# Kernel optimization log

Measured on AMD Instinct MI355X. Metric: run time of the kernel, lower is better.

The kernel has to match this reference:

```python
import jax, jax.numpy as jnp
import numpy as np

S = (128, 128, 128)  # spatial grid
K = (16, 16, 16)     # retained low-frequency modes


def _gelu(x):
    # torch nn.GELU default = exact erf variant
    return jax.nn.gelu(x, approximate=False)


def _flayer(x, Rr, Ri, w):
    # x: (s1,s2,s3,dv). Full rfftn then truncate to low modes (as in source).
    f = jnp.fft.rfftn(x, axes=(0, 1, 2))[: K[0], : K[1], : K[2]]  # (k1,k2,k3,dv) complex
    Rf = jnp.einsum('abcd,abcde->abce', f, Rr + 1j * Ri)           # per-mode channel mix
    kernelpart = jnp.fft.irfftn(Rf, s=S, axes=(0, 1, 2))           # zero-pad modes, back to grid
    return _gelu(kernelpart + x @ w)


def setup_inputs() -> dict:
    key = jax.random.key(0)
    ks = jax.random.split(key, 20)
    da, dv, dout = 4, 32, 1
    sc1, sc2, sc3 = 2.0 / da, 2.0 / dv, 2.0 / dv
    d = {}
    d['x'] = jax.random.normal(ks[0], (*S, da), dtype=jnp.float32)
    d['win'] = sc1 * jax.random.normal(ks[1], (da, dv), dtype=jnp.float32)
    d['bin1'] = sc1 * jax.random.normal(ks[2], (dv,), dtype=jnp.float32)
    i = 3
    for L in range(1, 5):
        d[f'Rphir{L}'] = sc2 * jax.random.normal(ks[i], (*K, dv, dv), dtype=jnp.float32); i += 1
        d[f'Rphii{L}'] = sc2 * jax.random.normal(ks[i], (*K, dv, dv), dtype=jnp.float32); i += 1
        d[f'w{L}'] = sc2 * jax.random.normal(ks[i], (dv, dv), dtype=jnp.float32); i += 1
    d['wout'] = sc3 * jax.random.normal(ks[i], (dv, dout), dtype=jnp.float32); i += 1
    d['bout'] = sc3 * jax.random.normal(ks[i], (dout,), dtype=jnp.float32)
    return d


def reference(x, win, bin1, Rphir1, Rphii1, w1, Rphir2, Rphii2, w2,
              Rphir3, Rphii3, w3, Rphir4, Rphii4, w4, wout, bout):
    v = _gelu(x @ win + bin1)          # lifting: (s1,s2,s3,dv)
    v = _flayer(v, Rphir1, Rphii1, w1)
    v = _flayer(v, Rphir2, Rphii2, w2)
    v = _flayer(v, Rphir3, Rphii3, w3)
    v = _flayer(v, Rphir4, Rphii4, w4)
    return v @ wout + bout             # (s1,s2,s3,dout)
```

## Files before the change

### kernel.cpp

```cpp
#include <hip/hip_runtime.h>
#include <math.h>

typedef float2 cplx;
typedef _Float16 h16;
typedef h16 h16x8 __attribute__((ext_vector_type(8)));
typedef float f32x4 __attribute__((ext_vector_type(4)));
typedef uint u32x2 __attribute__((ext_vector_type(2)));

#define MFMA16(a, b, c) __builtin_amdgcn_mfma_f32_16x16x32_f16(a, b, c, 0, 0, 0)

static __device__ __forceinline__ float gelu_exact(float z) {
  float x = z * 0.70710678118654752440f;
  float ax = fabsf(x);
  float t = __builtin_amdgcn_rcpf(fmaf(0.3275911f, ax, 1.0f));
  float p = fmaf(1.061405429f, t, -1.453152027f);
  p = fmaf(p, t, 1.421413741f);
  p = fmaf(p, t, -0.284496736f);
  p = fmaf(p, t, 0.254829592f);
  p = p * t;
  float e = __expf(-ax * ax);
  float erfax = fmaf(-p, e, 1.0f);
  float er = copysignf(erfax, x);
  return 0.5f * z * (1.0f + er);
}

template <int OFF>
static __device__ __forceinline__ h16x8 tr_frag(uint addr) {
  union { uint u[4]; h16x8 h; } r;
  u32x2 lo, hi;
  asm volatile("ds_read_b64_tr_b16 %0, %2 offset:%3\n\t"
               "ds_read_b64_tr_b16 %1, %2 offset:%4"
               : "=&v"(lo), "=&v"(hi)
               : "v"(addr), "i"(OFF), "i"(OFF + 128));
  r.u[0] = lo.x; r.u[1] = lo.y; r.u[2] = hi.x; r.u[3] = hi.y;
  return r.h;
}

__global__ __launch_bounds__(256) void k_prep(
    h16* __restrict__ Afwd, h16* __restrict__ Adt, cplx* __restrict__ Twc,
    const float* __restrict__ wA, const float* __restrict__ wB,
    const float* __restrict__ wC, h16* __restrict__ Wfr)
{
  const int tid = threadIdx.x;
  const float w0 = 0.049087385212340519f;
  for (int idx = tid; idx < 4096; idx += 256) {
    int Mt = idx >> 11, rem = idx & 2047, lane = rem >> 5, k = rem & 31;
    int j = k & 7, chunk = k >> 3;
    int m = lane & 15;
    int x3 = chunk * 32 + (lane >> 4) * 8 + j;
    float ang = (float)((m * x3) & 127) * w0;
    float s, c; sincosf(ang, &s, &c);
    float val = Mt ? s : c;
    h16 hi = (h16)val;
    Afwd[idx] = hi;
    Afwd[idx + 4096] = (h16)(val - (float)hi);
  }
  for (int idx = tid; idx < 4096; idx += 256) {
    int tt = idx >> 4, rem = idx & 15, t = rem >> 3, j = rem & 7;
    int wv = tt >> 6, lane = tt & 63, mrow = lane & 15, q = lane >> 4;
    int x3 = (2 * wv + t) * 16 + mrow;
    int kk = q * 8 + j;
    int m = (kk < 16) ? kk : kk - 16;
    float ang = (float)((x3 * m) & 127) * w0;
    float s, c; sincosf(ang, &s, &c);
    Adt[idx] = (h16)((kk < 16) ? c : s);
  }
  const float* ws[3] = { wA, wB, wC };
  for (int idx = tid; idx < 12288; idx += 256) {
    int L = idx >> 12, rem = idx & 4095;
    int t2 = rem >> 4, nt = (rem >> 3) & 1, j = rem & 7;
    int mrow = t2 & 15, q = (t2 >> 4) & 3;
    int n = nt * 16 + mrow, kk = q * 8 + j;
    Wfr[idx] = (h16)ws[L][kk * 32 + n];
  }
  if (tid < 128) {
    float ang = (float)tid * w0;
    float s, c; sincosf(ang, &s, &c);
    Twc[tid] = make_float2(c, s);
  }
}

__global__ __launch_bounds__(256) void k_lift(
    const float* __restrict__ x, const float* __restrict__ win,
    const float* __restrict__ bin, h16* __restrict__ v)
{
  __shared__ float xr[512];
  __shared__ float wl[128];
  __shared__ float bl[32];
  const int tid = threadIdx.x;
  const size_t b = blockIdx.x;
  const float* xrow = x + b * 512;
  for (int i = tid; i < 512; i += 256) xr[i] = xrow[i];
  if (tid < 128) wl[tid] = win[tid];
  if (tid < 32)  bl[tid] = bin[tid];
  __syncthreads();
  const int c = tid & 31, g = tid >> 5;
  #pragma unroll
  for (int j = 0; j < 16; ++j) {
    int x3 = g + 8 * j;
    float z = bl[c];
    #pragma unroll
    for (int a = 0; a < 4; ++a) z += xr[x3 * 4 + a] * wl[a * 32 + c];
    v[b * 4096 + x3 * 32 + c] = (h16)gelu_exact(z);
  }
}

__global__ __launch_bounds__(256) void k_fwd3(
    const h16* __restrict__ v, const h16* __restrict__ Afwd, cplx* __restrict__ Gp,
    const cplx* __restrict__ twg)
{
  __shared__ __align__(16) h16 vtile[4][2][4][32][16];
  __shared__ cplx F3L[4][512];
  __shared__ cplx twc[128];
  const int tid = threadIdx.x;
  const int x1 = blockIdx.x, qs = blockIdx.y;
  if (tid < 128) twc[tid] = twg[tid];
  const int lane = tid & 63, wv = tid >> 6;
  const int mrow = lane & 15, q4 = lane >> 4;
  h16x8 Ah[2][4], Al[2][4];
  #pragma unroll
  for (int Mt = 0; Mt < 2; ++Mt)
    #pragma unroll
    for (int ch = 0; ch < 4; ++ch) {
      Ah[Mt][ch] = *(const h16x8*)&Afwd[Mt * 2048 + lane * 32 + ch * 8];
      Al[Mt][ch] = *(const h16x8*)&Afwd[4096 + Mt * 2048 + lane * 32 + ch * 8];
    }
  const uint ldsbase = (uint)(uintptr_t)&vtile[0][0][0][0][0];
  const uint abase = ldsbase + (uint)(wv * 8192 + q4 * 256 + mrow * 2);
  cplx g0[16], g1[16];
  #pragma unroll
  for (int k2 = 0; k2 < 16; ++k2) { g0[k2] = make_float2(0.f, 0.f); g1[k2] = make_float2(0.f, 0.f); }
  for (int it = 0; it < 8; ++it) {
    const int x2b = qs * 32 + it * 4;
    __syncthreads();
    const uint4* vsrc = (const uint4*)(v + ((size_t)x1 * 128 + x2b) * 4096);
    for (int i = tid; i < 2048; i += 256) {
      uint4 pk = vsrc[i];
      int rr = i >> 9, e = (i & 511) * 8, x3 = e >> 5, c0 = e & 31;
      int panel = c0 >> 4, off = c0 & 15;
      int chunk = x3 >> 5, row = x3 & 31;
      *(uint4*)&vtile[rr][panel][chunk][row][off] = pk;
    }
    __syncthreads();
    h16x8 B0[4], B1[4];
    {
      const uint a0 = abase;
      const uint a1 = abase + 4096;
      B0[0] = tr_frag<0>(a0);    B0[1] = tr_frag<1024>(a0);
      B0[2] = tr_frag<2048>(a0); B0[3] = tr_frag<3072>(a0);
      B1[0] = tr_frag<0>(a1);    B1[1] = tr_frag<1024>(a1);
      B1[2] = tr_frag<2048>(a1); B1[3] = tr_frag<3072>(a1);
      asm volatile("s_waitcnt lgkmcnt(0)" ::: "memory");
      __builtin_amdgcn_sched_barrier(0);
    }
    f32x4 acc[2][2];
    #pragma unroll
    for (int Mt = 0; Mt < 2; ++Mt)
      #pragma unroll
      for (int Nt = 0; Nt < 2; ++Nt) acc[Mt][Nt] = (f32x4){0.f, 0.f, 0.f, 0.f};
    #pragma unroll
    for (int ch = 0; ch < 4; ++ch) {
      acc[0][0] = MFMA16(Ah[0][ch], B0[ch], acc[0][0]);
      acc[0][0] = MFMA16(Al[0][ch], B0[ch], acc[0][0]);
      acc[0][1] = MFMA16(Ah[0][ch], B1[ch], acc[0][1]);
      acc[0][1] = MFMA16(Al[0][ch], B1[ch], acc[0][1]);
      acc[1][0] = MFMA16(Ah[1][ch], B0[ch], acc[1][0]);
      acc[1][0] = MFMA16(Al[1][ch], B0[ch], acc[1][0]);
      acc[1][1] = MFMA16(Ah[1][ch], B1[ch], acc[1][1]);
      acc[1][1] = MFMA16(Al[1][ch], B1[ch], acc[1][1]);
    }
    #pragma unroll
    for (int Nt = 0; Nt < 2; ++Nt)
      #pragma unroll
      for (int r = 0; r < 4; ++r)
        F3L[wv][(q4 * 4 + r) * 32 + Nt * 16 + mrow] =
            make_float2(acc[0][Nt][r], -acc[1][Nt][r]);
    __syncthreads();
    #pragma unroll
    for (int rr = 0; rr < 4; ++rr) {
      const int x2 = x2b + rr;
      cplx f0 = F3L[rr][tid], f1 = F3L[rr][tid + 256];
      #pragma unroll
      for (int k2 = 0; k2 < 16; ++k2) {
        cplx t = twc[(k2 * x2) & 127];
        g0[k2].x += f0.x * t.x + f0.y * t.y;  g0[k2].y += f0.y * t.x - f0.x * t.y;
        g1[k2].x += f1.x * t.x + f1.y * t.y;  g1[k2].y += f1.y * t.x - f1.x * t.y;
      }
    }
  }
  cplx* dst = Gp + (size_t)qs * 1048576;
  #pragma unroll
  for (int k2 = 0; k2 < 16; ++k2) {
    size_t base = ((size_t)x1 * 16 + k2) * 512;
    dst[base + tid] = g0[k2];
    dst[base + 256 + tid] = g1[k2];
  }
}

__global__ __launch_bounds__(256) void k_spec(
    const cplx* __restrict__ Gp, const float* __restrict__ Rr,
    const float* __restrict__ Ri, cplx* __restrict__ H1,
    const cplx* __restrict__ twg)
{
  __shared__ cplx twc[128];
  __shared__ cplx fb[512];
  __shared__ cplx tb[512];
  const int tid = threadIdx.x;
  const int k2 = blockIdx.x >> 4, k3 = blockIdx.x & 15;
  if (tid < 128) twc[tid] = twg[tid];
  __syncthreads();
  const int c = tid & 31, g = tid >> 5;
  float fr0 = 0.f, fi0 = 0.f, fr1 = 0.f, fi1 = 0.f;
  for (int x1 = 0; x1 < 128; ++x1) {
    size_t idx = (((size_t)x1 * 16 + k2) * 16 + k3) * 32 + c;
    cplx p0 = Gp[idx], p1 = Gp[idx + 1048576], p2 = Gp[idx + 2097152], p3 = Gp[idx + 3145728];
    cplx h = make_float2(p0.x + p1.x + p2.x + p3.x, p0.y + p1.y + p2.y + p3.y);
    cplx ta = twc[(g * x1) & 127];
    cplx tb2 = twc[((g + 8) * x1) & 127];
    fr0 += h.x * ta.x + h.y * ta.y;   fi0 += h.y * ta.x - h.x * ta.y;
    fr1 += h.x * tb2.x + h.y * tb2.y; fi1 += h.y * tb2.x - h.x * tb2.y;
  }
  fb[g * 32 + c] = make_float2(fr0, fi0);
  fb[(g + 8) * 32 + c] = make_float2(fr1, fi1);
  __syncthreads();
  {
    const int e = c;
    float tr0 = 0.f, ti0 = 0.f, tr1 = 0.f, ti1 = 0.f;
    const size_t mb0 = ((size_t)g * 256 + k2 * 16 + k3) * 1024;
    const size_t mb1 = ((size_t)(g + 8) * 256 + k2 * 16 + k3) * 1024;
    #pragma unroll 4
    for (int cc = 0; cc < 32; ++cc) {
      float rr0 = Rr[mb0 + cc * 32 + e], ri0 = Ri[mb0 + cc * 32 + e];
      float rr1 = Rr[mb1 + cc * 32 + e], ri1 = Ri[mb1 + cc * 32 + e];
      cplx f0 = fb[g * 32 + cc], f1 = fb[(g + 8) * 32 + cc];
      tr0 += f0.x * rr0 - f0.y * ri0;  ti0 += f0.x * ri0 + f0.y * rr0;
      tr1 += f1.x * rr1 - f1.y * ri1;  ti1 += f1.x * ri1 + f1.y * rr1;
    }
    const float s = 4.76837158203125e-07f;
    tb[g * 32 + e] = make_float2(tr0 * s, ti0 * s);
    tb[(g + 8) * 32 + e] = make_float2(tr1 * s, ti1 * s);
  }
  __syncthreads();
  float trr[16], tii[16];
  #pragma unroll
  for (int k1 = 0; k1 < 16; ++k1) { cplx t = tb[k1 * 32 + c]; trr[k1] = t.x; tii[k1] = t.y; }
  #pragma unroll
  for (int j = 0; j < 16; ++j) {
    int xx1 = g + 8 * j;
    float hr = 0.f, hi = 0.f;
    #pragma unroll
    for (int k1 = 0; k1 < 16; ++k1) {
      cplx t = twc[(k1 * xx1) & 127];
      hr += trr[k1] * t.x - tii[k1] * t.y;
      hi += trr[k1] * t.y + tii[k1] * t.x;
    }
    H1[(((size_t)xx1 * 16 + k2) * 16 + k3) * 32 + c] = make_float2(hr, hi);
  }
}

__global__ __launch_bounds__(256) void k_ptm2(
    const cplx* __restrict__ H1, const h16* __restrict__ Wfr,
    h16* __restrict__ v, const h16* __restrict__ Adt,
    const cplx* __restrict__ twg)
{
  __shared__ __align__(16) h16 St[2][32 * 40];
  const int tid = threadIdx.x;
  const int x1 = blockIdx.y;
  const int x2b = blockIdx.x * 8;
  const int c = tid & 31, g = tid >> 5;
  const int lane = tid & 63, wv = tid >> 6;
  const int mrow = lane & 15, q = lane >> 4;
  h16x8 Adf[2], Bw[2];
  Adf[0] = *(const h16x8*)&Adt[tid * 16];
  Adf[1] = *(const h16x8*)&Adt[tid * 16 + 8];
  Bw[0]  = *(const h16x8*)&Wfr[tid * 16];
  Bw[1]  = *(const h16x8*)&Wfr[tid * 16 + 8];
  cplx h1a[16], h1b[16];
  {
    const cplx* h1p = H1 + (size_t)x1 * 8192;
    #pragma unroll
    for (int k2 = 0; k2 < 16; ++k2) {
      h1a[k2] = h1p[(k2 * 16 + g) * 32 + c];
      h1b[k2] = h1p[(k2 * 16 + g + 8) * 32 + c];
    }
  }
  for (int xi = 0; xi < 8; ++xi) {
    const int x2 = x2b + xi;
    const size_t b = (size_t)x1 * 128 + x2;
    h16x8 Av[2];
    #pragma unroll
    for (int t = 0; t < 2; ++t) {
      int x3 = (2 * wv + t) * 16 + mrow;
      Av[t] = *(const h16x8*)&v[b * 4096 + x3 * 32 + q * 8];
    }
    float r0 = 0.f, i0 = 0.f, r1 = 0.f, i1 = 0.f;
    #pragma unroll
    for (int k2 = 0; k2 < 16; ++k2) {
      cplx t = twg[(k2 * x2) & 127];
      r0 += h1a[k2].x * t.x - h1a[k2].y * t.y;  i0 += h1a[k2].x * t.y + h1a[k2].y * t.x;
      r1 += h1b[k2].x * t.x - h1b[k2].y * t.y;  i1 += h1b[k2].x * t.y + h1b[k2].y * t.x;
    }
    const float s0 = (g == 0) ? 1.f : 2.f;
    h16* stp = St[xi & 1];
    stp[c * 40 + g]      = (h16)(s0 * r0);
    stp[c * 40 + g + 8]  = (h16)(2.f * r1);
    stp[c * 40 + 16 + g] = (h16)(-s0 * i0);
    stp[c * 40 + 24 + g] = (h16)(-2.f * i1);
    __syncthreads();
    h16x8 Bst[2];
    #pragma unroll
    for (int nt = 0; nt < 2; ++nt)
      Bst[nt] = *(const h16x8*)&stp[(nt * 16 + mrow) * 40 + q * 8];
    f32x4 acc[2][2];
    #pragma unroll
    for (int t = 0; t < 2; ++t)
      #pragma unroll
      for (int nt = 0; nt < 2; ++nt) {
        f32x4 z = {0.f, 0.f, 0.f, 0.f};
        z = MFMA16(Adf[t], Bst[nt], z);
        z = MFMA16(Av[t], Bw[nt], z);
        acc[t][nt] = z;
      }
    #pragma unroll
    for (int t = 0; t < 2; ++t)
      #pragma unroll
      for (int nt = 0; nt < 2; ++nt)
        #pragma unroll
        for (int r = 0; r < 4; ++r) {
          int x3 = (2 * wv + t) * 16 + q * 4 + r;
          int cc = nt * 16 + mrow;
          v[b * 4096 + x3 * 32 + cc] = (h16)gelu_exact(acc[t][nt][r]);
        }
  }
}

__global__ __launch_bounds__(256) void k_ptf(
    const cplx* __restrict__ H1, const float* __restrict__ w,
    h16* __restrict__ v, const h16* __restrict__ Adt,
    const float* __restrict__ wout, const float* __restrict__ bout,
    float* __restrict__ out, const cplx* __restrict__ twg)
{
  __shared__ __align__(16) h16 vh[128 * 40];
  __shared__ __align__(16) h16 St[32 * 40];
  __shared__ __align__(16) h16 Wt[32 * 40];
  __shared__ cplx twc[128];
  __shared__ float wo[32];
  const int tid = threadIdx.x;
  const size_t b = blockIdx.x;
  const int x1 = (int)(b >> 7), x2 = (int)(b & 127);
  if (tid < 128) twc[tid] = twg[tid];
  {
    const uint* vg = (const uint*)(v + b * 4096);
    for (int i = tid; i < 2048; i += 256) {
      uint pk = vg[i];
      int e = 2 * i, r = e >> 5, cp = e & 31;
      *(uint*)&vh[r * 40 + cp] = pk;
    }
  }
  for (int i = tid; i < 1024; i += 256) {
    int k = i >> 5, n = i & 31;
    Wt[n * 40 + k] = (h16)w[i];
  }
  if (tid < 32) wo[tid] = wout[tid];
  __syncthreads();
  const int c = tid & 31, g = tid >> 5;
  {
    float r0 = 0.f, i0 = 0.f, r1 = 0.f, i1 = 0.f;
    const cplx* h1p = H1 + (size_t)x1 * 8192;
    #pragma unroll
    for (int k2 = 0; k2 < 16; ++k2) {
      cplx a  = h1p[(k2 * 16 + g) * 32 + c];
      cplx bb = h1p[(k2 * 16 + g + 8) * 32 + c];
      cplx t  = twc[(k2 * x2) & 127];
      r0 += a.x * t.x - a.y * t.y;   i0 += a.x * t.y + a.y * t.x;
      r1 += bb.x * t.x - bb.y * t.y; i1 += bb.x * t.y + bb.y * t.x;
    }
    const float s0 = (g == 0) ? 1.f : 2.f;
    St[c * 40 + g]        = (h16)(s0 * r0);
    St[c * 40 + g + 8]    = (h16)(2.f * r1);
    St[c * 40 + 16 + g]   = (h16)(-s0 * i0);
    St[c * 40 + 24 + g]   = (h16)(-2.f * i1);
  }
  const int lane = tid & 63, wv = tid >> 6;
  const int mrow = lane & 15, q = lane >> 4;
  h16x8 Adf[2];
  Adf[0] = *(const h16x8*)&Adt[tid * 16];
  Adf[1] = *(const h16x8*)&Adt[tid * 16 + 8];
  __syncthreads();
  h16x8 Bst[2], Bw[2], Av[2];
  #pragma unroll
  for (int nt = 0; nt < 2; ++nt) {
    int n = nt * 16 + mrow;
    Bst[nt] = *(const h16x8*)&St[n * 40 + q * 8];
    Bw[nt]  = *(const h16x8*)&Wt[n * 40 + q * 8];
  }
  #pragma unroll
  for (int t = 0; t < 2; ++t) {
    int x3 = (2 * wv + t) * 16 + mrow;
    Av[t] = *(const h16x8*)&vh[x3 * 40 + q * 8];
  }
  f32x4 acc[2][2];
  #pragma unroll
  for (int t = 0; t < 2; ++t)
    #pragma unroll
    for (int nt = 0; nt < 2; ++nt) {
      f32x4 z = {0.f, 0.f, 0.f, 0.f};
      z = MFMA16(Adf[t], Bst[nt], z);
      z = MFMA16(Av[t], Bw[nt], z);
      acc[t][nt] = z;
    }
  __syncthreads();
  #pragma unroll
  for (int t = 0; t < 2; ++t)
    #pragma unroll
    for (int nt = 0; nt < 2; ++nt)
      #pragma unroll
      for (int r = 0; r < 4; ++r) {
        int x3 = (2 * wv + t) * 16 + q * 4 + r;
        int cc = nt * 16 + mrow;
        vh[x3 * 40 + cc] = (h16)gelu_exact(acc[t][nt][r]);
      }
  __syncthreads();
  if (tid < 128) {
    float o = bout[0];
    #pragma unroll
    for (int cc = 0; cc < 32; ++cc) o += (float)vh[tid * 40 + cc] * wo[cc];
    out[b * 128 + tid] = o;
  }
}

__global__ void k_diag(float* out, float wsmb) {
  if (threadIdx.x == 0 && blockIdx.x == 0) out[0] = wsmb;
}

extern "C" void kernel_launch(void* const* d_in, const int* in_sizes, int n_in,
                              void* d_out, int out_size, void* d_ws, size_t ws_size,
                              hipStream_t stream)
{
  (void)in_sizes; (void)n_in; (void)out_size;
  const float* x    = (const float*)d_in[0];
  const float* win  = (const float*)d_in[1];
  const float* bin1 = (const float*)d_in[2];
  const float* Rr[4] = { (const float*)d_in[3], (const float*)d_in[6],
                         (const float*)d_in[9], (const float*)d_in[12] };
  const float* Ri[4] = { (const float*)d_in[4], (const float*)d_in[7],
                         (const float*)d_in[10], (const float*)d_in[13] };
  const float* wm[4] = { (const float*)d_in[5], (const float*)d_in[8],
                         (const float*)d_in[11], (const float*)d_in[14] };
  const float* wout = (const float*)d_in[15];
  const float* bout = (const float*)d_in[16];
  float* out = (float*)d_out;

  const size_t SZ_V  = 134217728;
  const size_t SZ_C  = 33554432;
  const size_t SZ_AF = 16384;
  const size_t SZ_AD = 8192;
  const size_t SZ_TW = 1024;
  const size_t SZ_WF = 24576;
  const size_t NEED = SZ_V + SZ_C + SZ_AF + SZ_AD + SZ_TW + SZ_WF;

  if (ws_size < NEED) {
    k_diag<<<1, 64, 0, stream>>>(out, (float)(ws_size >> 20));
    return;
  }
  char* p = (char*)d_ws;
  h16* v    = (h16*)p;  p += SZ_V;
  cplx* C   = (cplx*)p; p += SZ_C;
  h16* Afwd = (h16*)p;  p += SZ_AF;
  h16* Adt  = (h16*)p;  p += SZ_AD;
  cplx* Twc = (cplx*)p; p += SZ_TW;
  h16* Wfr  = (h16*)p;

  k_prep<<<1, 256, 0, stream>>>(Afwd, Adt, Twc, wm[0], wm[1], wm[2], Wfr);
  k_lift<<<16384, 256, 0, stream>>>(x, win, bin1, v);
  for (int L = 0; L < 4; ++L) {
    k_fwd3<<<dim3(128, 4), 256, 0, stream>>>(v, Afwd, C, Twc);
    k_spec<<<256, 256, 0, stream>>>(C, Rr[L], Ri[L], C, Twc);
    if (L < 3) k_ptm2<<<dim3(16, 128), 256, 0, stream>>>(C, Wfr + (size_t)L * 4096, v, Adt, Twc);
    else       k_ptf<<<16384, 256, 0, stream>>>(C, wm[3], v, Adt, wout, bout, out, Twc);
  }
}
```

Measured before the change: 848.1 us.

## Restructure final layer kernel to process eight rows per block with register-held spectra

The final pointwise/inverse-transform kernel now handles 8 x2 rows per block, loads the H1 spectral column into registers once, and reads v and the precomputed fp16 weight fragments directly from global memory instead of staging them through LDS. The output projection is fused into the MFMA epilogue through lane shuffles, which removes the LDS round-trip and two barriers. The launch grid drops from 16384 blocks to 2048. The spectral kernel's x1 loop also gets an unroll-4 pragma. The cost is higher register pressure and fewer, longer-running blocks.

```diff
diff --git a/kernel.cpp b/kernel.cpp
--- a/kernel.cpp
+++ b/kernel.cpp
@@ -39,7 +39,8 @@
 __global__ __launch_bounds__(256) void k_prep(
     h16* __restrict__ Afwd, h16* __restrict__ Adt, cplx* __restrict__ Twc,
     const float* __restrict__ wA, const float* __restrict__ wB,
-    const float* __restrict__ wC, h16* __restrict__ Wfr)
+    const float* __restrict__ wC, const float* __restrict__ wD,
+    h16* __restrict__ Wfr)
 {
   const int tid = threadIdx.x;
   const float w0 = 0.049087385212340519f;
@@ -65,8 +66,8 @@
     float s, c; sincosf(ang, &s, &c);
     Adt[idx] = (h16)((kk < 16) ? c : s);
   }
-  const float* ws[3] = { wA, wB, wC };
-  for (int idx = tid; idx < 12288; idx += 256) {
+  const float* ws[4] = { wA, wB, wC, wD };
+  for (int idx = tid; idx < 16384; idx += 256) {
     int L = idx >> 12, rem = idx & 4095;
     int t2 = rem >> 4, nt = (rem >> 3) & 1, j = rem & 7;
     int mrow = t2 & 15, q = (t2 >> 4) & 3;
@@ -211,6 +212,7 @@
   __syncthreads();
   const int c = tid & 31, g = tid >> 5;
   float fr0 = 0.f, fi0 = 0.f, fr1 = 0.f, fi1 = 0.f;
+  #pragma unroll 4
   for (int x1 = 0; x1 < 128; ++x1) {
     size_t idx = (((size_t)x1 * 16 + k2) * 16 + k3) * 32 + c;
     cplx p0 = Gp[idx], p1 = Gp[idx + 1048576], p2 = Gp[idx + 2097152], p3 = Gp[idx + 3145728];
@@ -334,98 +336,87 @@
   }
 }
 
-__global__ __launch_bounds__(256) void k_ptf(
-    const cplx* __restrict__ H1, const float* __restrict__ w,
-    h16* __restrict__ v, const h16* __restrict__ Adt,
+__global__ __launch_bounds__(256) void k_ptf2(
+    const cplx* __restrict__ H1, const h16* __restrict__ Wfr,
+    const h16* __restrict__ v, const h16* __restrict__ Adt,
     const float* __restrict__ wout, const float* __restrict__ bout,
     float* __restrict__ out, const cplx* __restrict__ twg)
 {
-  __shared__ __align__(16) h16 vh[128 * 40];
-  __shared__ __align__(16) h16 St[32 * 40];
-  __shared__ __align__(16) h16 Wt[32 * 40];
-  __shared__ cplx twc[128];
-  __shared__ float wo[32];
-  const int tid = threadIdx.x;
-  const size_t b = blockIdx.x;
-  const int x1 = (int)(b >> 7), x2 = (int)(b & 127);
-  if (tid < 128) twc[tid] = twg[tid];
-  {
-    const uint* vg = (const uint*)(v + b * 4096);
-    for (int i = tid; i < 2048; i += 256) {
-      uint pk = vg[i];
-      int e = 2 * i, r = e >> 5, cp = e & 31;
-      *(uint*)&vh[r * 40 + cp] = pk;
-    }
-  }
-  for (int i = tid; i < 1024; i += 256) {
-    int k = i >> 5, n = i & 31;
-    Wt[n * 40 + k] = (h16)w[i];
-  }
-  if (tid < 32) wo[tid] = wout[tid];
-  __syncthreads();
+  __shared__ __align__(16) h16 St[2][32 * 40];
+  const int tid = threadIdx.x;
+  const int x1 = blockIdx.y;
+  const int x2b = blockIdx.x * 8;
   const int c = tid & 31, g = tid >> 5;
-  {
-    float r0 = 0.f, i0 = 0.f, r1 = 0.f, i1 = 0.f;
-    const cplx* h1p = H1 + (size_t)x1 * 8192;
-    #pragma unroll
-    for (int k2 = 0; k2 < 16; ++k2) {
-      cplx a  = h1p[(k2 * 16 + g) * 32 + c];
-      cplx bb = h1p[(k2 * 16 + g + 8) * 32 + c];
-      cplx t  = twc[(k2 * x2) & 127];
-      r0 += a.x * t.x - a.y * t.y;   i0 += a.x * t.y + a.y * t.x;
-      r1 += bb.x * t.x - bb.y * t.y; i1 += bb.x * t.y + bb.y * t.x;
-    }
-    const float s0 = (g == 0) ? 1.f : 2.f;
-    St[c * 40 + g]        = (h16)(s0 * r0);
-    St[c * 40 + g + 8]    = (h16)(2.f * r1);
-    St[c * 40 + 16 + g]   = (h16)(-s0 * i0);
-    St[c * 40 + 24 + g]   = (h16)(-2.f * i1);
-  }
   const int lane = tid & 63, wv = tid >> 6;
   const int mrow = lane & 15, q = lane >> 4;
-  h16x8 Adf[2];
+  h16x8 Adf[2], Bw[2];
   Adf[0] = *(const h16x8*)&Adt[tid * 16];
   Adf[1] = *(const h16x8*)&Adt[tid * 16 + 8];
-  __syncthreads();
-  h16x8 Bst[2], Bw[2], Av[2];
-  #pragma unroll
-  for (int nt = 0; nt < 2; ++nt) {
-    int n = nt * 16 + mrow;
-    Bst[nt] = *(const h16x8*)&St[n * 40 + q * 8];
-    Bw[nt]  = *(const h16x8*)&Wt[n * 40 + q * 8];
-  }
-  #pragma unroll
-  for (int t = 0; t < 2; ++t) {
-    int x3 = (2 * wv + t) * 16 + mrow;
-    Av[t] = *(const h16x8*)&vh[x3 * 40 + q * 8];
-  }
-  f32x4 acc[2][2];
-  #pragma unroll
-  for (int t = 0; t < 2; ++t)
-    #pragma unroll
-    for (int nt = 0; nt < 2; ++nt) {
-      f32x4 z = {0.f, 0.f, 0.f, 0.f};
-      z = MFMA16(Adf[t], Bst[nt], z);
-      z = MFMA16(Av[t], Bw[nt], z);
-      acc[t][nt] = z;
-    }
-  __syncthreads();
-  #pragma unroll
-  for (int t = 0; t < 2; ++t)
+  Bw[0]  = *(const h16x8*)&Wfr[tid * 16];
+  Bw[1]  = *(const h16x8*)&Wfr[tid * 16 + 8];
+  const float wo0 = wout[mrow], wo1 = wout[16 + mrow];
+  const float bo = bout[0];
+  cplx h1a[16], h1b[16];
+  {
+    const cplx* h1p = H1 + (size_t)x1 * 8192;
+    #pragma unroll
+    for (int k2 = 0; k2 < 16; ++k2) {
+      h1a[k2] = h1p[(k2 * 16 + g) * 32 + c];
+      h1b[k2] = h1p[(k2 * 16 + g + 8) * 32 + c];
+    }
+  }
+  for (int xi = 0; xi < 8; ++xi) {
+    const int x2 = x2b + xi;
+    const size_t b = (size_t)x1 * 128 + x2;
+    h16x8 Av[2];
+    #pragma unroll
+    for (int t = 0; t < 2; ++t) {
+      int x3 = (2 * wv + t) * 16 + mrow;
+      Av[t] = *(const h16x8*)&v[b * 4096 + x3 * 32 + q * 8];
+    }
+    float r0 = 0.f, i0 = 0.f, r1 = 0.f, i1 = 0.f;
+    #pragma unroll
+    for (int k2 = 0; k2 < 16; ++k2) {
+      cplx t = twg[(k2 * x2) & 127];
+      r0 += h1a[k2].x * t.x - h1a[k2].y * t.y;  i0 += h1a[k2].x * t.y + h1a[k2].y * t.x;
+      r1 += h1b[k2].x * t.x - h1b[k2].y * t.y;  i1 += h1b[k2].x * t.y + h1b[k2].y * t.x;
+    }
+    const float s0 = (g == 0) ? 1.f : 2.f;
+    h16* stp = St[xi & 1];
+    stp[c * 40 + g]      = (h16)(s0 * r0);
+    stp[c * 40 + g + 8]  = (h16)(2.f * r1);
+    stp[c * 40 + 16 + g] = (h16)(-s0 * i0);
+    stp[c * 40 + 24 + g] = (h16)(-2.f * i1);
+    __syncthreads();
+    h16x8 Bst[2];
     #pragma unroll
     for (int nt = 0; nt < 2; ++nt)
+      Bst[nt] = *(const h16x8*)&stp[(nt * 16 + mrow) * 40 + q * 8];
+    f32x4 acc[2][2];
+    #pragma unroll
+    for (int t = 0; t < 2; ++t)
+      #pragma unroll
+      for (int nt = 0; nt < 2; ++nt) {
+        f32x4 z = {0.f, 0.f, 0.f, 0.f};
+        z = MFMA16(Adf[t], Bst[nt], z);
+        z = MFMA16(Av[t], Bw[nt], z);
+        acc[t][nt] = z;
+      }
+    #pragma unroll
+    for (int t = 0; t < 2; ++t)
       #pragma unroll
       for (int r = 0; r < 4; ++r) {
-        int x3 = (2 * wv + t) * 16 + q * 4 + r;
-        int cc = nt * 16 + mrow;
-        vh[x3 * 40 + cc] = (h16)gelu_exact(acc[t][nt][r]);
+        float p = (float)(h16)gelu_exact(acc[t][0][r]) * wo0
+                + (float)(h16)gelu_exact(acc[t][1][r]) * wo1;
+        p += __shfl_xor(p, 1);
+        p += __shfl_xor(p, 2);
+        p += __shfl_xor(p, 4);
+        p += __shfl_xor(p, 8);
+        if (mrow == 0) {
+          int x3 = (2 * wv + t) * 16 + q * 4 + r;
+          out[b * 128 + x3] = bo + p;
+        }
       }
-  __syncthreads();
-  if (tid < 128) {
-    float o = bout[0];
-    #pragma unroll
-    for (int cc = 0; cc < 32; ++cc) o += (float)vh[tid * 40 + cc] * wo[cc];
-    out[b * 128 + tid] = o;
   }
 }
 
@@ -456,7 +447,7 @@
   const size_t SZ_AF = 16384;
   const size_t SZ_AD = 8192;
   const size_t SZ_TW = 1024;
-  const size_t SZ_WF = 24576;
+  const size_t SZ_WF = 32768;
   const size_t NEED = SZ_V + SZ_C + SZ_AF + SZ_AD + SZ_TW + SZ_WF;
 
   if (ws_size < NEED) {
@@ -471,12 +462,12 @@
   cplx* Twc = (cplx*)p; p += SZ_TW;
   h16* Wfr  = (h16*)p;
 
-  k_prep<<<1, 256, 0, stream>>>(Afwd, Adt, Twc, wm[0], wm[1], wm[2], Wfr);
+  k_prep<<<1, 256, 0, stream>>>(Afwd, Adt, Twc, wm[0], wm[1], wm[2], wm[3], Wfr);
   k_lift<<<16384, 256, 0, stream>>>(x, win, bin1, v);
   for (int L = 0; L < 4; ++L) {
     k_fwd3<<<dim3(128, 4), 256, 0, stream>>>(v, Afwd, C, Twc);
     k_spec<<<256, 256, 0, stream>>>(C, Rr[L], Ri[L], C, Twc);
     if (L < 3) k_ptm2<<<dim3(16, 128), 256, 0, stream>>>(C, Wfr + (size_t)L * 4096, v, Adt, Twc);
-    else       k_ptf<<<16384, 256, 0, stream>>>(C, wm[3], v, Adt, wout, bout, out, Twc);
-  }
-}
+    else       k_ptf2<<<dim3(16, 128), 256, 0, stream>>>(C, Wfr + 3 * 4096, v, Adt, wout, bout, out, Twc);
+  }
+}
```

Measured after the change: 835.5 us. About the same (-1.5%).
